# Performance work log

Measured on AMD Instinct MI355X. Metric: run time of the kernel, lower is better.

Reference implementation:

```python
import math
import jax, jax.numpy as jnp
import numpy as np

B, C, L, EMB, ORDER = 4, 768, 8192, 33, 64


def setup_inputs() -> dict:
    key = jax.random.key(0)
    ks = jax.random.split(key, 8)
    x = jax.random.normal(ks[0], (B, C, L), jnp.float32)
    # 'batchias' param: jax.nn.initializers.normal() -> stddev 1e-2
    bias = 0.01 * jax.random.normal(ks[1], (C,), jnp.float32)
    # PositionalEmbedding z param (deterministic init)
    bands = (EMB - 1) // 2
    t_rescaled = jnp.linspace(0, L - 1, L)[None, :, None]
    w = 2 * math.pi * t_rescaled / L
    f = jnp.linspace(1e-4, bands - 1, bands)[None, None]
    zc = jnp.exp(-1j * f * w)
    time_emb = jnp.linspace(0, 1, L)[None, :, None]
    z = jnp.concatenate([time_emb, zc.real, zc.imag], axis=2).astype(jnp.float32)
    # ExponentialModulation deltas (deterministic init)
    target, fast_decay_pct, slow_decay_pct = 0.01, 0.3, 1.5
    max_decay = math.log(target) / fast_decay_pct
    min_decay = math.log(target) / slow_decay_pct
    deltas = jnp.linspace(min_decay, max_decay, C)[None, None].astype(jnp.float32)
    # implicit filter MLP params (Dense default lecun_normal-ish scale)
    def dense(k, fi, fo):
        return (jax.random.normal(k, (fi, fo), jnp.float32) / np.float32(np.sqrt(fi)))
    W0 = dense(ks[2], EMB, ORDER); b0 = jnp.zeros((ORDER,), jnp.float32)
    W1 = dense(ks[3], ORDER, ORDER); b1 = jnp.zeros((ORDER,), jnp.float32)
    W2 = dense(ks[4], ORDER, ORDER); b2 = jnp.zeros((ORDER,), jnp.float32)
    Wout = dense(ks[5], ORDER, C)  # no bias
    # Sin act constructed as Sin(dim=order) -> default freq=10, shared instance
    freq = 10.0 * jnp.ones((1, ORDER), jnp.float32)
    return dict(x=x, bias=bias, z=z, deltas=deltas, W0=W0, b0=b0, W1=W1, b1=b1,
                W2=W2, b2=b2, freq=freq, Wout=Wout, seq_len=L)


def _filter(z, deltas, W0, b0, W1, b1, W2, b2, freq, Wout, seq_len):
    # implicit MLP: (Dense -> Sin) x3, then Dense(num_channels, no bias)
    h = jnp.sin(freq * (z @ W0 + b0))
    h = jnp.sin(freq * (h @ W1 + b1))
    h = jnp.sin(freq * (h @ W2 + b2))
    h = h @ Wout  # [1, L, C]
    # exponential modulation: t = linspace(0,1,seq_len)
    t = jnp.linspace(0, 1, seq_len)[None, :, None]
    h = h * jnp.exp(-t * jnp.abs(deltas))
    return h


def _fft_conv(u, k, D):
    # u: [B, C, L], k: [C, L], D: [C]
    seq_len = u.shape[-1]
    fft_size = 2 * seq_len
    k_f = jnp.fft.rfft(k, n=fft_size) / fft_size
    u_f = jnp.fft.rfft(u, n=fft_size)
    y = jnp.fft.irfft(u_f * k_f, n=fft_size, norm='forward')[..., :seq_len]
    return (y + u * D[:, None]).astype(u.dtype)


def reference(x, bias, z, deltas, W0, b0, W1, b1, W2, b2, freq, Wout, seq_len):
    h = _filter(z, deltas, W0, b0, W1, b1, W2, b2, freq, Wout, seq_len)  # [1, L, C]
    k = h[0].T  # [C, L] (channel-major kernel as consumed by fft_conv)
    return _fft_conv(x, k, bias)
```

## Files before the change

### kernel.cpp

```cpp
#include <hip/hip_runtime.h>
#include <type_traits>
#include <utility>


typedef __attribute__((ext_vector_type(4))) short  short4v;
typedef __attribute__((ext_vector_type(8))) short  short8v;
typedef __attribute__((ext_vector_type(8))) __bf16 bf16x8;
typedef __attribute__((ext_vector_type(16))) float f32x16;

template <typename V, typename = void> struct MfmaTakes : std::false_type {};
template <typename V>
struct MfmaTakes<V, std::void_t<decltype(__builtin_amdgcn_mfma_f32_32x32x16_bf16(
    std::declval<V>(), std::declval<V>(), std::declval<f32x16>(), 0, 0, 0))>>
    : std::true_type {};

template <bool UseBf16> struct MfmaImpl;
template <> struct MfmaImpl<true> {
  template <typename V>
  static __device__ inline f32x16 run(V a, V b, f32x16 c) {
    return __builtin_amdgcn_mfma_f32_32x32x16_bf16(
        __builtin_bit_cast(bf16x8, a), __builtin_bit_cast(bf16x8, b), c, 0, 0, 0);
  }
};
template <> struct MfmaImpl<false> {
  template <typename V>
  static __device__ inline f32x16 run(V a, V b, f32x16 c) {
    return __builtin_amdgcn_mfma_f32_32x32x16_bf16(a, b, c, 0, 0, 0);
  }
};

__device__ inline f32x16 mfma_bf16(short8v a, short8v b, f32x16 c) {
  return MfmaImpl<MfmaTakes<bf16x8>::value>::run(a, b, c);
}

__device__ inline short8v pack8(short4v lo, short4v hi) {
  short8v v;
  v[0] = lo[0]; v[1] = lo[1]; v[2] = lo[2]; v[3] = lo[3];
  v[4] = hi[0]; v[5] = hi[1]; v[6] = hi[2]; v[7] = hi[3];
  return v;
}

__device__ inline short f2bf(float f) {
  unsigned int u = __builtin_bit_cast(unsigned int, f);
  u += 0x7FFFu + ((u >> 16) & 1u);
  return (short)(u >> 16);
}
__device__ inline float bf2f(short s) {
  unsigned int u = ((unsigned int)(unsigned short)s) << 16;
  return __builtin_bit_cast(float, u);
}

__global__ __launch_bounds__(256) void hyena_filter(
    const float* __restrict__ z, const float* __restrict__ deltas,
    const float* __restrict__ W0, const float* __restrict__ b0,
    const float* __restrict__ W1, const float* __restrict__ b1,
    const float* __restrict__ W2, const float* __restrict__ b2,
    const float* __restrict__ freq, const float* __restrict__ Wout,
    short* __restrict__ gk) {
  __shared__ float zt[32][33];
  __shared__ __align__(16) float hA[32][64];
  __shared__ __align__(16) float hB[32][64];
  const int tid = threadIdx.x;
  const int l0 = blockIdx.x << 5;

  for (int i = tid; i < 32 * 33; i += 256) {
    int l = i / 33, e = i - l * 33;
    zt[l][e] = z[(l0 + l) * 33 + e];
  }
  __syncthreads();
  for (int i = tid; i < 2048; i += 256) {
    int l = i >> 6, o = i & 63;
    float s = b0[o];
    for (int e = 0; e < 33; ++e) s += zt[l][e] * W0[e * 64 + o];
    hA[l][o] = sinf(freq[o] * s);
  }
  __syncthreads();
  for (int i = tid; i < 2048; i += 256) {
    int l = i >> 6, o = i & 63;
    float s = b1[o];
#pragma unroll
    for (int e = 0; e < 64; e += 4) {
      const float4 h4 = *reinterpret_cast<const float4*>(&hA[l][e]);
      s += h4.x * W1[e * 64 + o] + h4.y * W1[(e + 1) * 64 + o] +
           h4.z * W1[(e + 2) * 64 + o] + h4.w * W1[(e + 3) * 64 + o];
    }
    hB[l][o] = sinf(freq[o] * s);
  }
  __syncthreads();
  for (int i = tid; i < 2048; i += 256) {
    int l = i >> 6, o = i & 63;
    float s = b2[o];
#pragma unroll
    for (int e = 0; e < 64; e += 4) {
      const float4 h4 = *reinterpret_cast<const float4*>(&hB[l][e]);
      s += h4.x * W2[e * 64 + o] + h4.y * W2[(e + 1) * 64 + o] +
           h4.z * W2[(e + 2) * 64 + o] + h4.w * W2[(e + 3) * 64 + o];
    }
    hA[l][o] = sinf(freq[o] * s);
  }
  __syncthreads();
  {
    const int c0 = (blockIdx.y << 8) + tid;
    float a32[32];
#pragma unroll
    for (int l = 0; l < 32; ++l) a32[l] = 0.f;
    for (int o = 0; o < 64; o += 4) {
      const float w0 = Wout[(o + 0) * 768 + c0];
      const float w1 = Wout[(o + 1) * 768 + c0];
      const float w2 = Wout[(o + 2) * 768 + c0];
      const float w3 = Wout[(o + 3) * 768 + c0];
#pragma unroll
      for (int l = 0; l < 32; ++l) {
        const float4 h4 = *reinterpret_cast<const float4*>(&hA[l][o]);
        a32[l] += h4.x * w0 + h4.y * w1 + h4.z * w2 + h4.w * w3;
      }
    }
    const float del = fabsf(deltas[c0]);
    unsigned int* gku = reinterpret_cast<unsigned int*>(gk + (c0 << 13) + l0);
#pragma unroll
    for (int l = 0; l < 32; l += 2) {
      float t0 = (float)(l0 + l) * (1.f / 8191.f);
      float t1 = (float)(l0 + l + 1) * (1.f / 8191.f);
      unsigned short v0 = (unsigned short)f2bf(a32[l] * expf(-t0 * del));
      unsigned short v1 = (unsigned short)f2bf(a32[l + 1] * expf(-t1 * del));
      gku[l >> 1] = (unsigned int)v0 | ((unsigned int)v1 << 16);
    }
  }
}


#define ACC_ST(ACC, OFF)                                              \
  do {                                                                \
    _Pragma("unroll") for (int q = 0; q < 4; ++q) {                   \
      float4 v;                                                       \
      v.x = ACC[4 * q + 0]; v.y = ACC[4 * q + 1];                     \
      v.z = ACC[4 * q + 2]; v.w = ACC[4 * q + 3];                     \
      *reinterpret_cast<float4*>(sp + (OFF) + (q << 8)) = v;          \
    }                                                                 \
  } while (0)

#define ACC_LD(ACC, OFF)                                              \
  do {                                                                \
    _Pragma("unroll") for (int q = 0; q < 4; ++q) {                   \
      const float4 v =                                                \
          *reinterpret_cast<const float4*>(sp + (OFF) + (q << 8));    \
      ACC[4 * q + 0] += v.x; ACC[4 * q + 1] += v.y;                   \
      ACC[4 * q + 2] += v.z; ACC[4 * q + 3] += v.w;                   \
    }                                                                 \
  } while (0)

#define EPI(ACC, A)                                                   \
  do {                                                                \
    const int lb = lwb + ((A) << 8);                                  \
    _Pragma("unroll") for (int q = 0; q < 4; ++q) {                   \
      const int l0q = lb + (q << 3);                                  \
      const short4v xs =                                              \
          *reinterpret_cast<const short4v*>(&sXB[bcol][1008 + l0q]);  \
      float4 o4;                                                      \
      o4.x = ACC[4 * q + 0] + bc * bf2f(xs[0]);                       \
      o4.y = ACC[4 * q + 1] + bc * bf2f(xs[1]);                       \
      o4.z = ACC[4 * q + 2] + bc * bf2f(xs[2]);                       \
      o4.w = ACC[4 * q + 3] + bc * bf2f(xs[3]);                       \
      *reinterpret_cast<float4*>(out + obase + l0q) = o4;             \
    }                                                                 \
  } while (0)

__global__ __launch_bounds__(1024, 4) void hyena_conv(
    const float* __restrict__ x, const float* __restrict__ bias,
    const short* __restrict__ gk, float* __restrict__ out) {
  constexpr int LPAD = 1008;
  constexpr int XROW = 9224;
  __shared__ __align__(16) short sKR[4][8240];
  __shared__ __align__(16) short sXB[4][XROW];
  const int c = blockIdx.x;
  const int tid = threadIdx.x;

  for (int b = 0; b < 4; ++b) {
    const float* xr = x + ((b * 768 + c) << 13);
    for (int p = tid; p < XROW; p += 1024) {
      short v = 0;
      if (p >= LPAD && p < LPAD + 8192) v = f2bf(xr[p - LPAD]);
      sXB[b][p] = v;
    }
  }
  {
    const short* gkr = gk + (c << 13);
    for (int r = 0; r < 4; ++r)
      for (int u = tid; u < 8240; u += 1024) {
        int t = u + r;
        short v = 0;
        if (t >= 16 && t <= 8207) v = gkr[8207 - t];
        sKR[r][u] = v;
      }
  }
  __syncthreads();

  const int lane = tid & 63;
  const int wid  = tid >> 6;
  const int i31  = lane & 31;
  const int half = lane >> 5;
  const int base = half << 3;
  const int tcol = i31 >> 2;
  const int bcol = i31 & 3;
  const float bc = bias[c];

  const int j  = wid >> 1;
  const int t2 = ((j >> 2) << 1) | (j & 1);
  const int G  = (j & 2) ? (7 - t2) : t2;
  const int h  = wid & 1;
  const int NB = G + 1;
  const int lbase = G << 10;

  const int af0 = 8207 - i31 + base;
  const int rho = af0 & 3;
  const int u00 = af0 & ~3;
  const int pb  = LPAD + lbase + (tcol << 5) + base;
  const int d0  = (h * NB) << 9;

  const short* ka = &sKR[rho][0] + (u00 + 16 - d0);
  const short* xa = &sXB[bcol][0] + (pb + 16 - d0);

  f32x16 acc0, acc1, acc2, acc3;
#pragma unroll
  for (int r = 0; r < 16; ++r) {
    acc0[r] = 0.f; acc1[r] = 0.f; acc2[r] = 0.f; acc3[r] = 0.f;
  }

  for (int blk = 0; blk < NB; ++blk) {
#pragma unroll 2
    for (int t = 0; t < 16; ++t) {
      const short4v a0lo = *reinterpret_cast<const short4v*>(ka);
      const short4v a0hi = *reinterpret_cast<const short4v*>(ka + 4);
      const short4v a1lo = *reinterpret_cast<const short4v*>(ka - 256);
      const short4v a1hi = *reinterpret_cast<const short4v*>(ka - 252);
      const short8v A0 = pack8(a0lo, a0hi);
      const short8v A1 = pack8(a1lo, a1hi);
      const short8v Bm1 = *reinterpret_cast<const short8v*>(xa - 256);
      const short8v B0  = *reinterpret_cast<const short8v*>(xa);
      acc0 = mfma_bf16(A1, Bm1, acc0);
      acc0 = mfma_bf16(A0, B0, acc0);
      const short8v B1 = *reinterpret_cast<const short8v*>(xa + 256);
      acc1 = mfma_bf16(A1, B0, acc1);
      acc1 = mfma_bf16(A0, B1, acc1);
      const short8v B2 = *reinterpret_cast<const short8v*>(xa + 512);
      acc2 = mfma_bf16(A1, B1, acc2);
      acc2 = mfma_bf16(A0, B2, acc2);
      const short8v B3 = *reinterpret_cast<const short8v*>(xa + 768);
      acc3 = mfma_bf16(A1, B2, acc3);
      acc3 = mfma_bf16(A0, B3, acc3);
      ka -= 16; xa -= 16;
    }
    ka -= 256; xa -= 256;
  }

  __syncthreads();
  float* scr = reinterpret_cast<float*>(&sKR[0][0]);
  float* sp = scr + ((wid >> 1) << 11) + (lane << 2);
  if (h) { ACC_ST(acc0, 0); ACC_ST(acc1, 1024); }
  __syncthreads();
  if (!h) { ACC_LD(acc0, 0); ACC_LD(acc1, 1024); }
  __syncthreads();
  if (h) { ACC_ST(acc2, 0); ACC_ST(acc3, 1024); }
  __syncthreads();
  if (!h) {
    ACC_LD(acc2, 0); ACC_LD(acc3, 1024);
    const int obase = ((bcol * 768 + c) << 13);
    const int lwb = lbase + (tcol << 5) + (half << 2);
    EPI(acc0, 0); EPI(acc1, 1); EPI(acc2, 2); EPI(acc3, 3);
  }
}

extern "C" void kernel_launch(void* const* d_in, const int* in_sizes, int n_in,
                              void* d_out, int out_size, void* d_ws, size_t ws_size,
                              hipStream_t stream) {
  const float* x      = (const float*)d_in[0];
  const float* bias   = (const float*)d_in[1];
  const float* z      = (const float*)d_in[2];
  const float* deltas = (const float*)d_in[3];
  const float* W0     = (const float*)d_in[4];
  const float* b0     = (const float*)d_in[5];
  const float* W1     = (const float*)d_in[6];
  const float* b1     = (const float*)d_in[7];
  const float* W2     = (const float*)d_in[8];
  const float* b2     = (const float*)d_in[9];
  const float* freq   = (const float*)d_in[10];
  const float* Wout   = (const float*)d_in[11];
  float* out = (float*)d_out;
  short* gk = (short*)d_ws;

  hipLaunchKernelGGL(hyena_filter, dim3(256, 3), dim3(256), 0, stream,
                     z, deltas, W0, b0, W1, b1, W2, b2, freq, Wout, gk);
  hipLaunchKernelGGL(hyena_conv, dim3(768), dim3(1024), 0, stream,
                     x, bias, gk, out);
}
```

Measured before the change: 434.7 us.

## Rebalance conv work across waves with table-driven splits and coalesce filter stores

The conv kernel's per-wave work split changes from fixed G/half pairs to table-driven ranges [n0,n1) over 16-step units. Partial accumulators are reduced through shared-memory slots into owner waves, so the triangular causal workload is spread more evenly. The filter kernel now writes its output reversed and transposed through shared memory, giving coalesced 16-byte global stores, and the conv load reads it forward. The x staging also switches to vectorized float4 loads with bf16 packing. In exchange, the hardcoded tables make the wave schedule opaque and tied to these exact sizes.

Measured after the change: 407.1 us. 1.07x faster.

```diff
diff --git a/kernel.cpp b/kernel.cpp
--- a/kernel.cpp
+++ b/kernel.cpp
@@ -49,6 +49,13 @@
   unsigned int u = ((unsigned int)(unsigned short)s) << 16;
   return __builtin_bit_cast(float, u);
 }
+
+__device__ const unsigned char cGt[16]  = {2,7,4,6,1,7,4,6,5,7,3,6,3,0,5,5};
+__device__ const short         cN0[16]  = {0,0,0,0,0,86,80,75,0,171,64,150,0,0,64,128};
+__device__ const short         cN1[16]  = {96,86,80,75,64,171,160,150,64,256,128,224,64,32,128,192};
+__device__ const unsigned char cSLOT[16]= {255,255,255,255,255,0,1,2,255,3,4,5,255,255,6,7};
+__device__ const unsigned char cRA[16]  = {255,0,1,2,255,255,255,255,6,255,255,255,4,255,255,255};
+__device__ const unsigned char cRB[16]  = {255,3,255,5,255,255,255,255,7,255,255,255,255,255,255,255};
 
 __global__ __launch_bounds__(256) void hyena_filter(
     const float* __restrict__ z, const float* __restrict__ deltas,
@@ -60,6 +67,7 @@
   __shared__ float zt[32][33];
   __shared__ __align__(16) float hA[32][64];
   __shared__ __align__(16) float hB[32][64];
+  __shared__ __align__(16) unsigned int sT[256][20];
   const int tid = threadIdx.x;
   const int l0 = blockIdx.x << 5;
 
@@ -116,34 +124,50 @@
       }
     }
     const float del = fabsf(deltas[c0]);
-    unsigned int* gku = reinterpret_cast<unsigned int*>(gk + (c0 << 13) + l0);
-#pragma unroll
-    for (int l = 0; l < 32; l += 2) {
-      float t0 = (float)(l0 + l) * (1.f / 8191.f);
-      float t1 = (float)(l0 + l + 1) * (1.f / 8191.f);
-      unsigned short v0 = (unsigned short)f2bf(a32[l] * expf(-t0 * del));
-      unsigned short v1 = (unsigned short)f2bf(a32[l + 1] * expf(-t1 * del));
-      gku[l >> 1] = (unsigned int)v0 | ((unsigned int)v1 << 16);
-    }
-  }
-}
-
-
-#define ACC_ST(ACC, OFF)                                              \
+#pragma unroll
+    for (int l = 0; l < 32; ++l) {
+      const float t = (float)(l0 + l) * (1.f / 8191.f);
+      a32[l] *= expf(-t * del);
+    }
+#pragma unroll
+    for (int d = 0; d < 16; ++d) {
+      const unsigned int lo = (unsigned short)f2bf(a32[31 - 2 * d]);
+      const unsigned int hi = (unsigned short)f2bf(a32[30 - 2 * d]);
+      sT[tid][d] = lo | (hi << 16);
+    }
+  }
+  __syncthreads();
+  {
+    const int lane = tid & 63, wid = tid >> 6;
+    const int base_dw = 4080 - (blockIdx.x << 4);
+    unsigned int* gku = reinterpret_cast<unsigned int*>(gk);
+#pragma unroll
+    for (int q = 0; q < 4; ++q) {
+      const int r = (wid << 6) + (q << 4) + (lane >> 2);
+      const int m = (lane & 3) << 2;
+      const uint4 v = *reinterpret_cast<const uint4*>(&sT[r][m]);
+      const size_t cg = (size_t)((blockIdx.y << 8) + r);
+      *reinterpret_cast<uint4*>(gku + cg * 4096 + base_dw + m) = v;
+    }
+  }
+}
+
+
+#define ACC_ST(ACC, P, OFF)                                           \
   do {                                                                \
     _Pragma("unroll") for (int q = 0; q < 4; ++q) {                   \
       float4 v;                                                       \
       v.x = ACC[4 * q + 0]; v.y = ACC[4 * q + 1];                     \
       v.z = ACC[4 * q + 2]; v.w = ACC[4 * q + 3];                     \
-      *reinterpret_cast<float4*>(sp + (OFF) + (q << 8)) = v;          \
+      *reinterpret_cast<float4*>((P) + (OFF) + (q << 8)) = v;         \
     }                                                                 \
   } while (0)
 
-#define ACC_LD(ACC, OFF)                                              \
+#define ACC_LD(ACC, P, OFF)                                           \
   do {                                                                \
     _Pragma("unroll") for (int q = 0; q < 4; ++q) {                   \
       const float4 v =                                                \
-          *reinterpret_cast<const float4*>(sp + (OFF) + (q << 8));    \
+          *reinterpret_cast<const float4*>((P) + (OFF) + (q << 8));   \
       ACC[4 * q + 0] += v.x; ACC[4 * q + 1] += v.y;                   \
       ACC[4 * q + 2] += v.z; ACC[4 * q + 3] += v.w;                   \
     }                                                                 \
@@ -175,12 +199,21 @@
   const int c = blockIdx.x;
   const int tid = threadIdx.x;
 
-  for (int b = 0; b < 4; ++b) {
-    const float* xr = x + ((b * 768 + c) << 13);
-    for (int p = tid; p < XROW; p += 1024) {
-      short v = 0;
-      if (p >= LPAD && p < LPAD + 8192) v = f2bf(xr[p - LPAD]);
-      sXB[b][p] = v;
+  {
+    const short8v z8 = {0, 0, 0, 0, 0, 0, 0, 0};
+    for (int b = 0; b < 4; ++b) {
+      const float* xr = x + ((b * 768 + c) << 13);
+      if (tid < 126)
+        *reinterpret_cast<short8v*>(&sXB[b][tid << 3]) = z8;
+      if (tid >= 1021)
+        *reinterpret_cast<short8v*>(&sXB[b][9200 + ((tid - 1021) << 3)]) = z8;
+      const int s0 = tid << 3;
+      const float4 f0 = *reinterpret_cast<const float4*>(xr + s0);
+      const float4 f1 = *reinterpret_cast<const float4*>(xr + s0 + 4);
+      short8v v;
+      v[0] = f2bf(f0.x); v[1] = f2bf(f0.y); v[2] = f2bf(f0.z); v[3] = f2bf(f0.w);
+      v[4] = f2bf(f1.x); v[5] = f2bf(f1.y); v[6] = f2bf(f1.z); v[7] = f2bf(f1.w);
+      *reinterpret_cast<short8v*>(&sXB[b][LPAD + s0]) = v;
     }
   }
   {
@@ -189,7 +222,7 @@
       for (int u = tid; u < 8240; u += 1024) {
         int t = u + r;
         short v = 0;
-        if (t >= 16 && t <= 8207) v = gkr[8207 - t];
+        if (t >= 16 && t <= 8207) v = gkr[t - 16];
         sKR[r][u] = v;
       }
   }
@@ -204,18 +237,17 @@
   const int bcol = i31 & 3;
   const float bc = bias[c];
 
-  const int j  = wid >> 1;
-  const int t2 = ((j >> 2) << 1) | (j & 1);
-  const int G  = (j & 2) ? (7 - t2) : t2;
-  const int h  = wid & 1;
-  const int NB = G + 1;
+  const int G    = cGt[wid];
+  const int n0   = cN0[wid];
+  const int n1   = cN1[wid];
+  const int slot = cSLOT[wid];
   const int lbase = G << 10;
 
   const int af0 = 8207 - i31 + base;
   const int rho = af0 & 3;
   const int u00 = af0 & ~3;
   const int pb  = LPAD + lbase + (tcol << 5) + base;
-  const int d0  = (h * NB) << 9;
+  const int d0  = ((n0 >> 4) << 9) + ((n0 & 15) << 4);
 
   const short* ka = &sKR[rho][0] + (u00 + 16 - d0);
   const short* xa = &sXB[bcol][0] + (pb + 16 - d0);
@@ -226,44 +258,60 @@
     acc0[r] = 0.f; acc1[r] = 0.f; acc2[r] = 0.f; acc3[r] = 0.f;
   }
 
-  for (int blk = 0; blk < NB; ++blk) {
 #pragma unroll 2
-    for (int t = 0; t < 16; ++t) {
-      const short4v a0lo = *reinterpret_cast<const short4v*>(ka);
-      const short4v a0hi = *reinterpret_cast<const short4v*>(ka + 4);
-      const short4v a1lo = *reinterpret_cast<const short4v*>(ka - 256);
-      const short4v a1hi = *reinterpret_cast<const short4v*>(ka - 252);
-      const short8v A0 = pack8(a0lo, a0hi);
-      const short8v A1 = pack8(a1lo, a1hi);
-      const short8v Bm1 = *reinterpret_cast<const short8v*>(xa - 256);
-      const short8v B0  = *reinterpret_cast<const short8v*>(xa);
-      acc0 = mfma_bf16(A1, Bm1, acc0);
-      acc0 = mfma_bf16(A0, B0, acc0);
-      const short8v B1 = *reinterpret_cast<const short8v*>(xa + 256);
-      acc1 = mfma_bf16(A1, B0, acc1);
-      acc1 = mfma_bf16(A0, B1, acc1);
-      const short8v B2 = *reinterpret_cast<const short8v*>(xa + 512);
-      acc2 = mfma_bf16(A1, B1, acc2);
-      acc2 = mfma_bf16(A0, B2, acc2);
-      const short8v B3 = *reinterpret_cast<const short8v*>(xa + 768);
-      acc3 = mfma_bf16(A1, B2, acc3);
-      acc3 = mfma_bf16(A0, B3, acc3);
-      ka -= 16; xa -= 16;
-    }
-    ka -= 256; xa -= 256;
+  for (int n = n0; n < n1; ++n) {
+    const short4v a0lo = *reinterpret_cast<const short4v*>(ka);
+    const short4v a0hi = *reinterpret_cast<const short4v*>(ka + 4);
+    const short4v a1lo = *reinterpret_cast<const short4v*>(ka - 256);
+    const short4v a1hi = *reinterpret_cast<const short4v*>(ka - 252);
+    const short8v A0 = pack8(a0lo, a0hi);
+    const short8v A1 = pack8(a1lo, a1hi);
+    const short8v Bm1 = *reinterpret_cast<const short8v*>(xa - 256);
+    const short8v B0  = *reinterpret_cast<const short8v*>(xa);
+    acc0 = mfma_bf16(A1, Bm1, acc0);
+    acc0 = mfma_bf16(A0, B0, acc0);
+    const short8v B1 = *reinterpret_cast<const short8v*>(xa + 256);
+    acc1 = mfma_bf16(A1, B0, acc1);
+    acc1 = mfma_bf16(A0, B1, acc1);
+    const short8v B2 = *reinterpret_cast<const short8v*>(xa + 512);
+    acc2 = mfma_bf16(A1, B1, acc2);
+    acc2 = mfma_bf16(A0, B2, acc2);
+    const short8v B3 = *reinterpret_cast<const short8v*>(xa + 768);
+    acc3 = mfma_bf16(A1, B2, acc3);
+    acc3 = mfma_bf16(A0, B3, acc3);
+    const int dec = 16 + (((n & 15) == 15) << 8);
+    ka -= dec; xa -= dec;
   }
 
   __syncthreads();
   float* scr = reinterpret_cast<float*>(&sKR[0][0]);
-  float* sp = scr + ((wid >> 1) << 11) + (lane << 2);
-  if (h) { ACC_ST(acc0, 0); ACC_ST(acc1, 1024); }
-  __syncthreads();
-  if (!h) { ACC_LD(acc0, 0); ACC_LD(acc1, 1024); }
-  __syncthreads();
-  if (h) { ACC_ST(acc2, 0); ACC_ST(acc3, 1024); }
-  __syncthreads();
-  if (!h) {
-    ACC_LD(acc2, 0); ACC_LD(acc3, 1024);
+  const int isOwner = (slot == 255);
+  float* sp = scr + (isOwner ? 0 : slot * 2048) + (lane << 2);
+  const int ra = cRA[wid], rb = cRB[wid];
+  if (!isOwner) { ACC_ST(acc0, sp, 0); ACC_ST(acc1, sp, 1024); }
+  __syncthreads();
+  if (isOwner) {
+    if (ra != 255) {
+      float* lp = scr + ra * 2048 + (lane << 2);
+      ACC_LD(acc0, lp, 0); ACC_LD(acc1, lp, 1024);
+    }
+    if (rb != 255) {
+      float* lp = scr + rb * 2048 + (lane << 2);
+      ACC_LD(acc0, lp, 0); ACC_LD(acc1, lp, 1024);
+    }
+  }
+  __syncthreads();
+  if (!isOwner) { ACC_ST(acc2, sp, 0); ACC_ST(acc3, sp, 1024); }
+  __syncthreads();
+  if (isOwner) {
+    if (ra != 255) {
+      float* lp = scr + ra * 2048 + (lane << 2);
+      ACC_LD(acc2, lp, 0); ACC_LD(acc3, lp, 1024);
+    }
+    if (rb != 255) {
+      float* lp = scr + rb * 2048 + (lane << 2);
+      ACC_LD(acc2, lp, 0); ACC_LD(acc3, lp, 1024);
+    }
     const int obase = ((bcol * 768 + c) << 13);
     const int lwb = lbase + (tcol << 5) + (half << 2);
     EPI(acc0, 0); EPI(acc1, 1); EPI(acc2, 2); EPI(acc3, 3);
```
